# Optimization experiments

Hardware: AMD Instinct MI355X
Metric: run time of the kernel (lower is better)

## Reference

```python
import jax, jax.numpy as jnp
import numpy as np

B, T, S, H = 8, 256, 256, 512

def setup_inputs() -> dict:
    key = jax.random.key(0)
    k1, k2, k3, k4, k5, k6 = jax.random.split(key, 6)
    query = jax.random.normal(k1, (B, T, H), dtype=jnp.float32)
    encoder_outputs = jax.random.normal(k2, (B, S, H), dtype=jnp.float32)
    # lengths in [1, S] so every row has at least one valid source position
    src_lengths = jax.random.randint(k3, (B,), 1, S + 1, dtype=jnp.int64)
    scale = 1.0 / np.sqrt(H)
    W_h = jax.random.normal(k4, (H, H), dtype=jnp.float32) * scale  # nn.Linear weight (out, in)
    W_s = jax.random.normal(k5, (H, H), dtype=jnp.float32) * scale
    v = jax.random.normal(k6, (H,), dtype=jnp.float32) * scale     # nn.Linear(H,1) weight squeezed
    return {"query": query, "encoder_outputs": encoder_outputs,
            "src_lengths": src_lengths, "W_h": W_h, "W_s": W_s, "v": v}

def reference(query, encoder_outputs, src_lengths, W_h, W_s, v):
    # Linear without bias: y = x @ W^T
    enc_f = jnp.einsum('bsh,oh->bso', encoder_outputs, W_h)   # (B,S,H)
    qry_f = jnp.einsum('bth,oh->bto', query, W_s)             # (B,T,H)
    # additive score: v^T tanh(enc_f + qry_f), broadcast over (T,S)
    scores = jnp.einsum('btsh,h->bts',
                        jnp.tanh(enc_f[:, None, :, :] + qry_f[:, :, None, :]), v)  # (B,T,S)
    mask = jnp.arange(S)[None, :] >= src_lengths[:, None]      # (B,S) True = pad
    scores = jnp.where(mask[:, None, :], -jnp.inf, scores)
    attn_weights = jax.nn.softmax(scores, axis=-1)             # (B,T,S)
    attn_out = jnp.einsum('bts,bsh->bth', attn_weights, encoder_outputs)
    return attn_out
```

## Files before the change

kernel.cpp:

```cpp
#include <hip/hip_runtime.h>
#include <hip/hip_cooperative_groups.h>
#include <cstddef>
#include <math.h>

namespace cg = cooperative_groups;

#define BD 8
#define TD 256
#define SD 256
#define HD 512
#define K2F 2.885390081777927f

#define EXP2(x) __builtin_amdgcn_exp2f(x)
#define RCP(x)  __builtin_amdgcn_rcpf(x)

typedef __attribute__((ext_vector_type(8))) _Float16 half8;
typedef __attribute__((ext_vector_type(4))) _Float16 half4;
typedef __attribute__((ext_vector_type(4))) float float4v;

__device__ __forceinline__ float exp2_sat(float x) {
    return EXP2(fminf(fmaxf(x, -80.0f), 80.0f));
}

#define LSTR 40

__device__ __forceinline__ void phaseA(
    int bid, int tid, float* smem,
    const float* __restrict__ enc, const float* __restrict__ qry,
    const float* __restrict__ Wh,  const float* __restrict__ Ws,
    float* __restrict__ encT, float* __restrict__ qryf)
{
    const int l  = tid & 63;
    const int w  = tid >> 6;
    const int rf = l & 15;
    const int q  = l >> 4;

    _Float16* LA = (_Float16*)smem;
    _Float16* LB = (_Float16*)(smem + 1280);

    const int x  = bid & 7;
    const int k  = bid >> 3;
    const bool isq = k >= 32;
    const int kk = k & 31;
    const int my = (isq ? 32 : 0) + x * 4 + (kk & 3);
    const int n0 = (kk >> 2) * 64;
    const int m0 = my * 64;

    const int srow = tid >> 3;
    const int scol = (tid & 7) * 4;
    const float* Abase = isq
        ? qry + (size_t)(m0 - 2048 + srow) * HD + scol
        : enc + (size_t)(m0 + srow) * HD + scol;
    const float* Bbase = (isq ? Ws : Wh) + (size_t)(n0 + srow) * HD + scol;

    const int mi = (w & 3) * 16;
    const int ni = (w >> 2) * 32;

    float4v acc[2] = {{0,0,0,0},{0,0,0,0}};

    float4 a0 = *(const float4*)(Abase);
    float4 b0 = *(const float4*)(Bbase);

    for (int ks = 0; ks < 16; ++ks) {
        if (ks) __syncthreads();
        {
            half4 ha, hb;
            ha[0]=(_Float16)a0.x; ha[1]=(_Float16)a0.y; ha[2]=(_Float16)a0.z; ha[3]=(_Float16)a0.w;
            hb[0]=(_Float16)b0.x; hb[1]=(_Float16)b0.y; hb[2]=(_Float16)b0.z; hb[3]=(_Float16)b0.w;
            *(half4*)&LA[srow * LSTR + scol] = ha;
            *(half4*)&LB[srow * LSTR + scol] = hb;
        }
        __syncthreads();
        if (ks + 1 < 16) {
            const int ko = (ks + 1) * 32;
            a0 = *(const float4*)(Abase + ko);
            b0 = *(const float4*)(Bbase + ko);
        }
        half8 ah = *(const half8*)&LA[(mi + rf) * LSTR + q * 8];
        #pragma unroll
        for (int j = 0; j < 2; ++j) {
            half8 bh = *(const half8*)&LB[(ni + j * 16 + rf) * LSTR + q * 8];
            acc[j] = __builtin_amdgcn_mfma_f32_16x16x32_f16(ah, bh, acc[j], 0, 0, 0);
        }
    }

    if (!isq) {
        const int b  = m0 >> 8;
        const int sb = (m0 & 255) + mi + q * 4;
        float* base = encT + (size_t)b * HD * SD;
        #pragma unroll
        for (int j = 0; j < 2; ++j) {
            float4 o = make_float4(exp2_sat(acc[j][0]*K2F), exp2_sat(acc[j][1]*K2F),
                                   exp2_sat(acc[j][2]*K2F), exp2_sat(acc[j][3]*K2F));
            *(float4*)(base + (size_t)(n0 + ni + j * 16 + rf) * SD + sb) = o;
        }
    } else {
        const int mrow = (m0 - 2048) + mi + q * 4;
        #pragma unroll
        for (int j = 0; j < 2; ++j)
            #pragma unroll
            for (int r = 0; r < 4; ++r)
                qryf[(size_t)(mrow + r) * HD + n0 + ni + j * 16 + rf] =
                    exp2_sat(acc[j][r] * K2F);
    }
}

template<int TT>
__device__ __forceinline__ void phaseB(
    int b, int t0, int tid, float* smem,
    const float* __restrict__ enc, const float* __restrict__ encT,
    const float* __restrict__ qryf, const float* __restrict__ v,
    const int* __restrict__ lens, float* __restrict__ out)
{
    const int l = tid & 63;
    const int w = tid >> 6;

    float* qls = smem;
    float* pls = smem + 512 * TT;
    float* wls = smem + 1536 * TT;

    {
        const float* qf = qryf + ((size_t)b * TD + t0) * HD;
        #pragma unroll
        for (int t = 0; t < TT; ++t) qls[tid * TT + t] = qf[t * HD + tid];
    }
    __syncthreads();

    float a[TT][4];
    #pragma unroll
    for (int t = 0; t < TT; ++t)
        #pragma unroll
        for (int c = 0; c < 4; ++c) a[t][c] = 0.0f;
    {
        const float* ep = encT + (size_t)b * HD * SD + (size_t)(w * 64) * SD + l * 4;
        const int jbase = w * 64;
        #pragma unroll 4
        for (int jj = 0; jj < 64; ++jj) {
            float4 e = *(const float4*)(ep + (size_t)jj * SD);
            float vj = v[jbase + jj];
            float qv[TT];
            #pragma unroll
            for (int t = 0; t < TT; ++t) qv[t] = qls[(jbase + jj) * TT + t];
            float ev[4] = {e.x, e.y, e.z, e.w};
            #pragma unroll
            for (int t = 0; t < TT; ++t)
                #pragma unroll
                for (int c = 0; c < 4; ++c) {
                    float p = fmaf(ev[c], qv[t], 1.0f);
                    a[t][c] = fmaf(vj, RCP(p), a[t][c]);
                }
        }
    }
    if (w < 4) {
        #pragma unroll
        for (int t = 0; t < TT; ++t)
            *(float4*)&pls[(w * TT + t) * 256 + l * 4] =
                make_float4(a[t][0], a[t][1], a[t][2], a[t][3]);
    }
    __syncthreads();
    if (w >= 4) {
        #pragma unroll
        for (int t = 0; t < TT; ++t) {
            float4 c4 = *(const float4*)&pls[((w - 4) * TT + t) * 256 + l * 4];
            c4.x += a[t][0]; c4.y += a[t][1]; c4.z += a[t][2]; c4.w += a[t][3];
            *(float4*)&pls[((w - 4) * TT + t) * 256 + l * 4] = c4;
        }
    }
    __syncthreads();

    if (w < TT) {
        const int t = w;
        float p[4] = {0, 0, 0, 0};
        #pragma unroll
        for (int g = 0; g < 4; ++g) {
            float4 pp = *(const float4*)&pls[(g * TT + t) * 256 + l * 4];
            p[0] += pp.x; p[1] += pp.y; p[2] += pp.z; p[3] += pp.w;
        }
        const int len = lens[b];
        const int s0 = l * 4;
        float sc[4];
        #pragma unroll
        for (int c = 0; c < 4; ++c)
            sc[c] = (s0 + c < len) ? -2.0f * p[c] : -INFINITY;
        float mx = fmaxf(fmaxf(sc[0], sc[1]), fmaxf(sc[2], sc[3]));
        #pragma unroll
        for (int off = 32; off; off >>= 1) mx = fmaxf(mx, __shfl_xor(mx, off));
        float ex[4]; float sum = 0.0f;
        #pragma unroll
        for (int c = 0; c < 4; ++c) { ex[c] = __expf(sc[c] - mx); sum += ex[c]; }
        #pragma unroll
        for (int off = 32; off; off >>= 1) sum += __shfl_xor(sum, off);
        const float inv = RCP(sum);
        *(float4*)&wls[t * SD + s0] = make_float4(ex[0]*inv, ex[1]*inv, ex[2]*inv, ex[3]*inv);
    }
    __syncthreads();

    const int sg = tid >> 7;
    const int h4 = (tid & 127) * 4;
    float* avred = pls;
    float4 o[TT];
    #pragma unroll
    for (int t = 0; t < TT; ++t) o[t] = make_float4(0.f, 0.f, 0.f, 0.f);
    {
        const float* eb = enc + (size_t)b * SD * HD + h4;
        #pragma unroll 2
        for (int ss = 0; ss < 64; ++ss) {
            const int s = sg * 64 + ss;
            float4 evv = *(const float4*)(eb + (size_t)s * HD);
            float wt[TT];
            #pragma unroll
            for (int t = 0; t < TT; ++t) wt[t] = wls[t * SD + s];
            #pragma unroll
            for (int t = 0; t < TT; ++t) {
                o[t].x = fmaf(wt[t], evv.x, o[t].x);
                o[t].y = fmaf(wt[t], evv.y, o[t].y);
                o[t].z = fmaf(wt[t], evv.z, o[t].z);
                o[t].w = fmaf(wt[t], evv.w, o[t].w);
            }
        }
    }
    if (sg < 2) {
        #pragma unroll
        for (int t = 0; t < TT; ++t)
            *(float4*)&avred[(size_t)(sg * TT + t) * 512 + h4] = o[t];
    }
    __syncthreads();
    if (sg >= 2) {
        #pragma unroll
        for (int t = 0; t < TT; ++t) {
            float4 c4 = *(const float4*)&avred[(size_t)((sg - 2) * TT + t) * 512 + h4];
            c4.x += o[t].x; c4.y += o[t].y; c4.z += o[t].z; c4.w += o[t].w;
            *(float4*)&avred[(size_t)((sg - 2) * TT + t) * 512 + h4] = c4;
        }
    }
    __syncthreads();

    if (tid < TT * 128) {
        const int t  = tid >> 7;
        const int hh = (tid & 127) * 4;
        float4 x0 = *(const float4*)&avred[(size_t)(0 * TT + t) * 512 + hh];
        float4 x1 = *(const float4*)&avred[(size_t)(1 * TT + t) * 512 + hh];
        float4 r = make_float4(x0.x + x1.x, x0.y + x1.y, x0.z + x1.z, x0.w + x1.w);
        *(float4*)(out + ((size_t)b * TD + t0 + t) * HD + hh) = r;
    }
}

__global__ __launch_bounds__(512) void fused1024(
    const float* __restrict__ enc, const float* __restrict__ qry,
    const float* __restrict__ Wh,  const float* __restrict__ Ws,
    const float* __restrict__ v,   const int* __restrict__ lens,
    float* __restrict__ encT, float* __restrict__ qryf, float* __restrict__ out)
{
    __shared__ float smem[3584];
    const int bid = blockIdx.x;
    if (bid < 512)
        phaseA(bid, threadIdx.x, smem, enc, qry, Wh, Ws, encT, qryf);
    cg::this_grid().sync();
    phaseB<2>(bid & 7, (bid >> 3) * 2, threadIdx.x, smem,
              enc, encT, qryf, v, lens, out);
}

__global__ __launch_bounds__(512) void fused512(
    const float* __restrict__ enc, const float* __restrict__ qry,
    const float* __restrict__ Wh,  const float* __restrict__ Ws,
    const float* __restrict__ v,   const int* __restrict__ lens,
    float* __restrict__ encT, float* __restrict__ qryf, float* __restrict__ out)
{
    __shared__ float smem[7168];
    const int bid = blockIdx.x;
    phaseA(bid, threadIdx.x, smem, enc, qry, Wh, Ws, encT, qryf);
    cg::this_grid().sync();
    phaseB<4>(bid & 7, (bid >> 3) * 4, threadIdx.x, smem,
              enc, encT, qryf, v, lens, out);
}

__global__ __launch_bounds__(256) void proj_fb(
    const float* __restrict__ enc, const float* __restrict__ qry,
    const float* __restrict__ Wh,  const float* __restrict__ Ws,
    float* __restrict__ encT, float* __restrict__ qryf)
{
    __shared__ _Float16 LA[64 * LSTR], LB[64 * LSTR];

    const int tid = threadIdx.x;
    const int l = tid & 63, w = tid >> 6;
    const int rf = l & 15, q = l >> 4;
    const int my = blockIdx.y;
    const bool isq = my >= 32;
    const int m0 = my * 64;
    const int n0 = blockIdx.x * 64;

    const int srow = tid >> 2;
    const int scol = (tid & 3) * 8;
    const float* Abase = isq
        ? qry + (size_t)(m0 - 2048 + srow) * HD + scol
        : enc + (size_t)(m0 + srow) * HD + scol;
    const float* Bbase = (isq ? Ws : Wh) + (size_t)(n0 + srow) * HD + scol;

    const int mi = (w & 1) * 32, ni = (w >> 1) * 32;
    float4v acc[2][2] = {{{0,0,0,0},{0,0,0,0}},{{0,0,0,0},{0,0,0,0}}};

    float4 a0 = *(const float4*)(Abase);
    float4 a1 = *(const float4*)(Abase + 4);
    float4 b0 = *(const float4*)(Bbase);
    float4 b1 = *(const float4*)(Bbase + 4);

    for (int ks = 0; ks < 16; ++ks) {
        if (ks) __syncthreads();
        {
            float af[8] = {a0.x,a0.y,a0.z,a0.w,a1.x,a1.y,a1.z,a1.w};
            float bf[8] = {b0.x,b0.y,b0.z,b0.w,b1.x,b1.y,b1.z,b1.w};
            half8 ha, hb;
            #pragma unroll
            for (int i = 0; i < 8; ++i) { ha[i] = (_Float16)af[i]; hb[i] = (_Float16)bf[i]; }
            *(half8*)&LA[srow * LSTR + scol] = ha;
            *(half8*)&LB[srow * LSTR + scol] = hb;
        }
        __syncthreads();
        if (ks + 1 < 16) {
            const int ko = (ks + 1) * 32;
            a0 = *(const float4*)(Abase + ko);
            a1 = *(const float4*)(Abase + ko + 4);
            b0 = *(const float4*)(Bbase + ko);
            b1 = *(const float4*)(Bbase + ko + 4);
        }
        half8 ah[2], bh[2];
        #pragma unroll
        for (int i = 0; i < 2; ++i) {
            ah[i] = *(const half8*)&LA[(mi + i * 16 + rf) * LSTR + q * 8];
            bh[i] = *(const half8*)&LB[(ni + i * 16 + rf) * LSTR + q * 8];
        }
        #pragma unroll
        for (int i = 0; i < 2; ++i)
            #pragma unroll
            for (int j = 0; j < 2; ++j)
                acc[i][j] = __builtin_amdgcn_mfma_f32_16x16x32_f16(ah[i], bh[j], acc[i][j], 0, 0, 0);
    }

    if (!isq) {
        const int b  = m0 >> 8;
        const int sb = (m0 & 255) + mi + q * 4;
        float* base = encT + (size_t)b * HD * SD;
        #pragma unroll
        for (int i = 0; i < 2; ++i)
            #pragma unroll
            for (int j = 0; j < 2; ++j) {
                float4 o = make_float4(exp2_sat(acc[i][j][0]*K2F), exp2_sat(acc[i][j][1]*K2F),
                                       exp2_sat(acc[i][j][2]*K2F), exp2_sat(acc[i][j][3]*K2F));
                *(float4*)(base + (size_t)(n0 + ni + j * 16 + rf) * SD + sb + i * 16) = o;
            }
    } else {
        const int mrow = (m0 - 2048) + mi + q * 4;
        #pragma unroll
        for (int i = 0; i < 2; ++i)
            #pragma unroll
            for (int j = 0; j < 2; ++j)
                #pragma unroll
                for (int r = 0; r < 4; ++r)
                    qryf[(size_t)(mrow + i * 16 + r) * HD + n0 + ni + j * 16 + rf] =
                        exp2_sat(acc[i][j][r] * K2F);
    }
}

__global__ __launch_bounds__(512) void attn_fb(
    const float* __restrict__ enc, const float* __restrict__ encT,
    const float* __restrict__ qryf, const float* __restrict__ v,
    const int* __restrict__ lens, float* __restrict__ out)
{
    __shared__ float qls[HD * 4];
    __shared__ float pls[8 * 4 * 256];
    __shared__ float wls[4 * SD];

    const int blk = blockIdx.x;
    const int b   = blk >> 6;
    const int t0  = (blk & 63) * 4;
    const int tid = threadIdx.x;
    const int w   = tid >> 6;
    const int l   = tid & 63;

    {
        const float* qf = qryf + ((size_t)b * TD + t0) * HD;
        float4 qv;
        qv.x = qf[0 * HD + tid]; qv.y = qf[1 * HD + tid];
        qv.z = qf[2 * HD + tid]; qv.w = qf[3 * HD + tid];
        *(float4*)&qls[tid * 4] = qv;
    }
    __syncthreads();

    float a[4][4];
    #pragma unroll
    for (int t = 0; t < 4; ++t)
        #pragma unroll
        for (int c = 0; c < 4; ++c) a[t][c] = 0.0f;
    {
        const float* ep = encT + (size_t)b * HD * SD + (size_t)(w * 64) * SD + l * 4;
        const int jbase = w * 64;
        #pragma unroll 4
        for (int jj = 0; jj < 64; ++jj) {
            float4 e = *(const float4*)(ep + (size_t)jj * SD);
            float4 q4 = *(const float4*)&qls[(jbase + jj) * 4];
            float vj = v[jbase + jj];
            float ev[4] = {e.x, e.y, e.z, e.w};
            float qv[4] = {q4.x, q4.y, q4.z, q4.w};
            #pragma unroll
            for (int t = 0; t < 4; ++t)
                #pragma unroll
                for (int c = 0; c < 4; ++c) {
                    float p = fmaf(ev[c], qv[t], 1.0f);
                    a[t][c] = fmaf(vj, RCP(p), a[t][c]);
                }
        }
    }
    #pragma unroll
    for (int t = 0; t < 4; ++t)
        *(float4*)&pls[(w * 4 + t) * 256 + l * 4] = make_float4(a[t][0], a[t][1], a[t][2], a[t][3]);
    __syncthreads();

    if (w < 4) {
        const int t = w;
        float p[4] = {0, 0, 0, 0};
        #pragma unroll
        for (int g = 0; g < 8; ++g) {
            float4 pp = *(const float4*)&pls[(g * 4 + t) * 256 + l * 4];
            p[0] += pp.x; p[1] += pp.y; p[2] += pp.z; p[3] += pp.w;
        }
        const int len = lens[b];
        const int s0 = l * 4;
        float sc[4];
        #pragma unroll
        for (int c = 0; c < 4; ++c)
            sc[c] = (s0 + c < len) ? -2.0f * p[c] : -INFINITY;
        float mx = fmaxf(fmaxf(sc[0], sc[1]), fmaxf(sc[2], sc[3]));
        #pragma unroll
        for (int off = 32; off; off >>= 1) mx = fmaxf(mx, __shfl_xor(mx, off));
        float ex[4]; float sum = 0.0f;
        #pragma unroll
        for (int c = 0; c < 4; ++c) { ex[c] = __expf(sc[c] - mx); sum += ex[c]; }
        #pragma unroll
        for (int off = 32; off; off >>= 1) sum += __shfl_xor(sum, off);
        const float inv = RCP(sum);
        *(float4*)&wls[t * SD + s0] = make_float4(ex[0]*inv, ex[1]*inv, ex[2]*inv, ex[3]*inv);
    }
    __syncthreads();

    const int g  = tid >> 7;
    const int h4 = (tid & 127) * 4;
    float* avred = pls;
    {
        const float* eb = enc + (size_t)b * SD * HD + h4;
        float4 o[4] = {{0,0,0,0},{0,0,0,0},{0,0,0,0},{0,0,0,0}};
        #pragma unroll 2
        for (int ss = 0; ss < 64; ++ss) {
            const int s = g * 64 + ss;
            float4 evv = *(const float4*)(eb + (size_t)s * HD);
            float wt[4];
            #pragma unroll
            for (int t = 0; t < 4; ++t) wt[t] = wls[t * SD + s];
            #pragma unroll
            for (int t = 0; t < 4; ++t) {
                o[t].x = fmaf(wt[t], evv.x, o[t].x);
                o[t].y = fmaf(wt[t], evv.y, o[t].y);
                o[t].z = fmaf(wt[t], evv.z, o[t].z);
                o[t].w = fmaf(wt[t], evv.w, o[t].w);
            }
        }
        #pragma unroll
        for (int t = 0; t < 4; ++t)
            *(float4*)&avred[(size_t)(g * 4 + t) * 512 + h4] = o[t];
    }
    __syncthreads();
    {
        const int t  = tid >> 7;
        const int hh = (tid & 127) * 4;
        float4 r = {0, 0, 0, 0};
        #pragma unroll
        for (int gg = 0; gg < 4; ++gg) {
            float4 x = *(const float4*)&avred[(size_t)(gg * 4 + t) * 512 + hh];
            r.x += x.x; r.y += x.y; r.z += x.z; r.w += x.w;
        }
        *(float4*)(out + ((size_t)b * TD + t0 + t) * HD + hh) = r;
    }
}

extern "C" void kernel_launch(void* const* d_in, const int* in_sizes, int n_in,
                              void* d_out, int out_size, void* d_ws, size_t ws_size,
                              hipStream_t stream) {
    const float* query = (const float*)d_in[0];
    const float* enc   = (const float*)d_in[1];
    const int*   lens  = (const int*)d_in[2];
    const float* W_h   = (const float*)d_in[3];
    const float* W_s   = (const float*)d_in[4];
    const float* v     = (const float*)d_in[5];
    float* out = (float*)d_out;

    char* ws = (char*)d_ws;
    float* encT = (float*)(ws);
    float* qryf = (float*)(ws + ((size_t)4 << 20));

    void* args[] = {
        (void*)&enc, (void*)&query, (void*)&W_h, (void*)&W_s,
        (void*)&v, (void*)&lens, (void*)&encT, (void*)&qryf, (void*)&out
    };

    int nb = 0;
    hipError_t oerr = hipOccupancyMaxActiveBlocksPerMultiprocessor(
        &nb, (const void*)fused1024, 512, 0);
    if (oerr == hipSuccess && nb >= 4) {
        hipError_t lerr = hipLaunchCooperativeKernel((const void*)fused1024,
                                                     dim3(1024), dim3(512), args, 0, stream);
        if (lerr == hipSuccess) return;
    }

    nb = 0;
    oerr = hipOccupancyMaxActiveBlocksPerMultiprocessor(
        &nb, (const void*)fused512, 512, 0);
    if (oerr == hipSuccess && nb >= 2) {
        hipError_t lerr = hipLaunchCooperativeKernel((const void*)fused512,
                                                     dim3(512), dim3(512), args, 0, stream);
        if (lerr == hipSuccess) return;
    }

    dim3 pgrid(HD / 64, 64);
    proj_fb<<<pgrid, 256, 0, stream>>>(enc, query, W_h, W_s, encT, qryf);
    attn_fb<<<BD * (TD / 4), 512, 0, stream>>>(enc, encT, qryf, v, lens, out);
}
```

Before: 120.8 us.

## Use 512 cooperative blocks of 1024 threads with all-block projection phase

Replaces the 1024-block by 512-thread cooperative kernel with 512 blocks of 1024 threads. A new projection routine gives every block one 64x64 output tile, computed by 16 waves using 16x16x32 f16 MFMA, so no block sits idle during the projection phase as half of them did before. In the attention phase each block runs two 512-thread halves, each on its own region of shared memory. The intent is a cheaper grid-wide sync over fewer blocks and better use of the GPU during projection. The risks are register pressure from the launch_bounds(1024, 8) hint and the single-buffered k-loop, which adds two block-wide barriers per step.

```diff
diff --git a/kernel.cpp b/kernel.cpp
--- a/kernel.cpp
+++ b/kernel.cpp
@@ -105,6 +105,73 @@
     }
 }
 
+__device__ __forceinline__ void phaseA1024(
+    int bid, int tid, float* smem,
+    const float* __restrict__ enc, const float* __restrict__ qry,
+    const float* __restrict__ Wh,  const float* __restrict__ Ws,
+    float* __restrict__ encT, float* __restrict__ qryf)
+{
+    const int l  = tid & 63;
+    const int w  = tid >> 6;
+    const int rf = l & 15;
+    const int q  = l >> 4;
+
+    _Float16* LA = (_Float16*)smem;
+    _Float16* LB = (_Float16*)(smem + 1280);
+
+    const int x  = bid & 7;
+    const int k  = bid >> 3;
+    const bool isq = k >= 32;
+    const int kk = k & 31;
+    const int my = (isq ? 32 : 0) + x * 4 + (kk & 3);
+    const int n0 = (kk >> 2) * 64;
+    const int m0 = my * 64;
+
+    const bool stagesA = (tid < 512);
+    const int srow = (tid >> 3) & 63;
+    const int scol = (tid & 7) * 4;
+    const float* Sbase = stagesA
+        ? (isq ? qry + (size_t)(m0 - 2048 + srow) * HD
+               : enc + (size_t)(m0 + srow) * HD) + scol
+        : (isq ? Ws : Wh) + (size_t)(n0 + srow) * HD + scol;
+    _Float16* Ldst = (stagesA ? LA : LB) + srow * LSTR + scol;
+
+    const int mi = (w & 3) * 16;
+    const int ni = (w >> 2) * 16;
+
+    float4v acc = {0, 0, 0, 0};
+
+    float4 a0 = *(const float4*)(Sbase);
+
+    for (int ks = 0; ks < 16; ++ks) {
+        if (ks) __syncthreads();
+        {
+            half4 ha;
+            ha[0]=(_Float16)a0.x; ha[1]=(_Float16)a0.y; ha[2]=(_Float16)a0.z; ha[3]=(_Float16)a0.w;
+            *(half4*)Ldst = ha;
+        }
+        __syncthreads();
+        if (ks + 1 < 16) a0 = *(const float4*)(Sbase + (ks + 1) * 32);
+        half8 ah = *(const half8*)&LA[(mi + rf) * LSTR + q * 8];
+        half8 bh = *(const half8*)&LB[(ni + rf) * LSTR + q * 8];
+        acc = __builtin_amdgcn_mfma_f32_16x16x32_f16(ah, bh, acc, 0, 0, 0);
+    }
+
+    if (!isq) {
+        const int b  = m0 >> 8;
+        const int sb = (m0 & 255) + mi + q * 4;
+        float* base = encT + (size_t)b * HD * SD;
+        float4 o = make_float4(exp2_sat(acc[0]*K2F), exp2_sat(acc[1]*K2F),
+                               exp2_sat(acc[2]*K2F), exp2_sat(acc[3]*K2F));
+        *(float4*)(base + (size_t)(n0 + ni + rf) * SD + sb) = o;
+    } else {
+        const int mrow = (m0 - 2048) + mi + q * 4;
+        #pragma unroll
+        for (int r = 0; r < 4; ++r)
+            qryf[(size_t)(mrow + r) * HD + n0 + ni + rf] = exp2_sat(acc[r] * K2F);
+    }
+}
+
 template<int TT>
 __device__ __forceinline__ void phaseB(
     int b, int t0, int tid, float* smem,
@@ -245,18 +312,23 @@
     }
 }
 
-__global__ __launch_bounds__(512) void fused1024(
+__global__ __launch_bounds__(1024, 8) void fusedT(
     const float* __restrict__ enc, const float* __restrict__ qry,
     const float* __restrict__ Wh,  const float* __restrict__ Ws,
     const float* __restrict__ v,   const int* __restrict__ lens,
     float* __restrict__ encT, float* __restrict__ qryf, float* __restrict__ out)
 {
-    __shared__ float smem[3584];
+    __shared__ float smem[7168];
     const int bid = blockIdx.x;
-    if (bid < 512)
-        phaseA(bid, threadIdx.x, smem, enc, qry, Wh, Ws, encT, qryf);
+    const int tid = threadIdx.x;
+
+    phaseA1024(bid, tid, smem, enc, qry, Wh, Ws, encT, qryf);
+
     cg::this_grid().sync();
-    phaseB<2>(bid & 7, (bid >> 3) * 2, threadIdx.x, smem,
+
+    const int sub  = tid >> 9;
+    const int stid = tid & 511;
+    phaseB<2>(bid & 7, (bid >> 3) * 4 + sub * 2, stid, smem + sub * 3584,
               enc, encT, qryf, v, lens, out);
 }
 
@@ -503,10 +575,10 @@
 
     int nb = 0;
     hipError_t oerr = hipOccupancyMaxActiveBlocksPerMultiprocessor(
-        &nb, (const void*)fused1024, 512, 0);
-    if (oerr == hipSuccess && nb >= 4) {
-        hipError_t lerr = hipLaunchCooperativeKernel((const void*)fused1024,
-                                                     dim3(1024), dim3(512), args, 0, stream);
+        &nb, (const void*)fusedT, 1024, 0);
+    if (oerr == hipSuccess && nb >= 2) {
+        hipError_t lerr = hipLaunchCooperativeKernel((const void*)fusedT,
+                                                     dim3(512), dim3(1024), args, 0, stream);
         if (lerr == hipSuccess) return;
     }
 
```

Measured after the change: 121.8 us. No clear change (+0.8%).
